# Kernel optimization log

Measured on AMD Instinct MI355X. Metric: run time of the kernel, lower is better.

## Reference

```python
import jax, jax.numpy as jnp
import numpy as np

EPS = 1e-05  # epsilon from __init__
K, D = 2048, 256  # codebook_size, embed dim (hardcoded in module)
B, T = 8, 8192


def setup_inputs() -> dict:
    key = jax.random.key(0)
    k1, k2, k3 = jax.random.split(key, 3)
    hidden_states = jax.random.normal(k1, (B, T, D), dtype=jnp.float32)
    embed_sum = jax.random.normal(k2, (K, D), dtype=jnp.float32)
    # cluster_usage starts as ones in the module; use positive random counts
    cluster_usage = jax.random.uniform(k3, (K,), dtype=jnp.float32) * 10.0 + 0.5
    return {"hidden_states": hidden_states, "embed_sum": embed_sum, "cluster_usage": cluster_usage}


def reference(hidden_states, embed_sum, cluster_usage):
    # embed property: embed_sum / clamp(cluster_usage, min=eps)[:, None]
    embed = embed_sum / jnp.clip(cluster_usage, EPS, None)[:, None]  # [K, D]

    shape = hidden_states.shape
    x = hidden_states.reshape(-1, shape[-1]).astype(jnp.float32)  # [N, D]

    x2 = jnp.sum(x * x, axis=-1, keepdims=True)        # [N, 1]
    e2 = jnp.sum(embed * embed, axis=-1)               # [K]
    d2 = x2 - 2.0 * (x @ embed.T) + e2[None, :]        # [N, K] -- the big intermediate

    embed_ind = jnp.argmin(d2, axis=-1).reshape(shape[:-1])  # [B, T]
    # decode: embedding lookup of selected codes
    quantized = jnp.take(embed, embed_ind, axis=0)            # [B, T, D]
    return embed_ind, quantized
```

## Files before the change

### kernel.cpp

```cpp
#include <hip/hip_runtime.h>
#include <hip/hip_bf16.h>


typedef float f32x4 __attribute__((ext_vector_type(4)));
typedef short s16x8 __attribute__((ext_vector_type(8)));

#define D_DIM 256
#define N_ROWS 65536
#define K_CODES 2048
#define VQ_EPS 1e-5f
#define DELTA 0.5f

__device__ __forceinline__ short bf16s(float f) {
    __hip_bfloat16 h = __float2bfloat16(f);
    return __builtin_bit_cast(short, h);
}
__device__ __forceinline__ unsigned fkey(float f) {
    unsigned u = __float_as_uint(f);
    return u ^ (unsigned)(((int)u >> 31) | (int)0x80000000);
}
__device__ __forceinline__ float funkey(unsigned k) {
    unsigned u = (k & 0x80000000u) ? (k ^ 0x80000000u) : ~k;
    return __uint_as_float(u);
}
__device__ __forceinline__ void gload16(const void* g, void* l) {
    __builtin_amdgcn_global_load_lds(
        (const __attribute__((address_space(1))) void*)g,
        (__attribute__((address_space(3))) void*)l, 16, 0, 0);
}

__device__ __forceinline__ void np_sumsq_16lane(const float* a, float* out, int g) {
#pragma clang fp contract(off)
    int j = g & 7, h = g >> 3;
    const float* p = a + h * 128;
    float t = p[j];
    float r = t * t;
#pragma unroll
    for (int i = 1; i < 16; ++i) { float v = p[j + 8 * i]; r += v * v; }
    r += __shfl_xor(r, 1);
    r += __shfl_xor(r, 2);
    r += __shfl_xor(r, 4);
    float other = __shfl_xor(r, 8);
    if (g == 0) *out = r + other;
}

__global__ void prep_codebook(const float* __restrict__ es, const float* __restrict__ us,
                              float* __restrict__ embed, unsigned short* __restrict__ eswz,
                              float* __restrict__ e2) {
    __shared__ float le[8][256];
    const int tid = threadIdx.x;
    const int rloc = tid >> 5, idx = tid & 31;
    const int r = blockIdx.x * 8 + rloc;
    const float u = fmaxf(us[r], VQ_EPS);
    f32x4 v0 = *(const f32x4*)&es[r * D_DIM + idx * 8];
    f32x4 v1 = *(const f32x4*)&es[r * D_DIM + idx * 8 + 4];
    f32x4 e0, e1;
#pragma unroll
    for (int j = 0; j < 4; ++j) { e0[j] = v0[j] / u; e1[j] = v1[j] / u; }
    *(f32x4*)&embed[r * D_DIM + idx * 8] = e0;
    *(f32x4*)&embed[r * D_DIM + idx * 8 + 4] = e1;
    *(f32x4*)&le[rloc][idx * 8] = e0;
    *(f32x4*)&le[rloc][idx * 8 + 4] = e1;
    int kc = idx >> 2, ss = idx & 3;
    int sd = ss ^ ((r >> 1) & 3);
    s16x8 b;
#pragma unroll
    for (int j = 0; j < 4; ++j) { b[j] = bf16s(e0[j]); b[j + 4] = bf16s(e1[j]); }
    *(s16x8*)&eswz[r * 256 + kc * 32 + sd * 8] = b;
    __syncthreads();
    if (idx < 16) np_sumsq_16lane(&le[rloc][0], &e2[r], idx);
}

__global__ void prep_x(const float* __restrict__ x, unsigned short* __restrict__ dst,
                       float* __restrict__ x2) {
    int gid = blockIdx.x * 256 + threadIdx.x;
    int r = gid >> 5, idx = gid & 31;
    int kc = idx >> 2, s = idx & 3;
    int k0 = kc * 32 + (s ^ ((r >> 1) & 3)) * 8;
    const float* p = x + r * D_DIM + k0;
    s16x8 v;
#pragma unroll
    for (int j = 0; j < 8; ++j) v[j] = bf16s(p[j]);
    *(s16x8*)&dst[r * 256 + kc * 32 + s * 8] = v;
    if (idx < 16)
        np_sumsq_16lane(x + r * D_DIM, x2 + r, idx);
}

__launch_bounds__(256, 2)
__global__ void vq_scan(const unsigned short* __restrict__ xswz,
                        const unsigned short* __restrict__ eswz,
                        const float* __restrict__ e2, const float* __restrict__ x2,
                        unsigned* __restrict__ keys1, unsigned* __restrict__ keys2) {
    __shared__ __align__(16) short lds[2][2][4096];

    const int bid = blockIdx.x;
    const int swz = (bid & 7) * 1024 + (bid >> 3);
    const int mt = swz >> 4, nt = swz & 15;
    const int m_base = mt * 128, n_base = nt * 128;
    const int tid = threadIdx.x, lane = tid & 63, wid = tid >> 6;
    const int rb = wid * 32;
    const int l15 = lane & 15, lg = lane >> 4;

    f32x4 acc[2][8];
#pragma unroll
    for (int m = 0; m < 2; ++m)
#pragma unroll
        for (int n = 0; n < 8; ++n) { f32x4 z = {0.f, 0.f, 0.f, 0.f}; acc[m][n] = z; }

    auto stage = [&](int buf, int kc) {
#pragma unroll
        for (int i = 0; i < 2; ++i) {
            int off = i * 4096 + wid * 1024 + lane * 16;
            int row = off >> 6, slot = (off >> 4) & 3;
            gload16((const char*)xswz + (((size_t)(m_base + row)) << 9) + (kc << 6) + (slot << 4),
                    (char*)&lds[buf][0][0] + off);
            gload16((const char*)eswz + (((size_t)(n_base + row)) << 9) + (kc << 6) + (slot << 4),
                    (char*)&lds[buf][1][0] + off);
        }
    };
    auto compute = [&](int buf) {
        const short* A = &lds[buf][0][0];
        const short* B = &lds[buf][1][0];
        s16x8 af[2], bf[8];
#pragma unroll
        for (int m = 0; m < 2; ++m) {
            int R = rb + m * 16 + l15, s = lg ^ ((R >> 1) & 3);
            af[m] = *(const s16x8*)&A[R * 32 + s * 8];
        }
#pragma unroll
        for (int n = 0; n < 8; ++n) {
            int R = n * 16 + l15, s = lg ^ ((R >> 1) & 3);
            bf[n] = *(const s16x8*)&B[R * 32 + s * 8];
        }
#pragma unroll
        for (int m = 0; m < 2; ++m)
#pragma unroll
            for (int n = 0; n < 8; ++n)
                acc[m][n] = __builtin_amdgcn_mfma_f32_16x16x32_bf16(af[m], bf[n], acc[m][n], 0, 0, 0);
    };

    stage(0, 0);
    __syncthreads();
#pragma unroll 1
    for (int kc = 0; kc < 8; ++kc) {
        if (kc < 7) stage((kc + 1) & 1, kc + 1);
        compute(kc & 1);
        __syncthreads();
    }

    const int grow0 = m_base + rb + lg * 4;
    float e2v[8];
#pragma unroll
    for (int n = 0; n < 8; ++n) e2v[n] = e2[n_base + n * 16 + l15];

#pragma unroll
    for (int m = 0; m < 2; ++m) {
#pragma unroll
        for (int j = 0; j < 4; ++j) {
            int gr = grow0 + m * 16 + j;
            float x2v = x2[gr];
            unsigned k1 = 0xFFFFFFFFu, k2 = 0xFFFFFFFFu;
#pragma unroll
            for (int n = 0; n < 8; ++n) {
                float d2 = (x2v - 2.0f * acc[m][n][j]) + e2v[n];
                unsigned pk = (fkey(d2) & 0xFFFFF800u)
                              | (unsigned)(n_base + n * 16 + l15);
                unsigned lo = pk < k1 ? pk : k1;
                unsigned hi = pk < k1 ? k1 : pk;
                k2 = hi < k2 ? hi : k2;
                k1 = lo;
            }
#pragma unroll
            for (int s = 1; s < 16; s <<= 1) {
                unsigned o1 = __shfl_xor(k1, s);
                unsigned o2 = __shfl_xor(k2, s);
                unsigned lo = o1 < k1 ? o1 : k1;
                unsigned hi = o1 < k1 ? k1 : o1;
                unsigned m2 = o2 < k2 ? o2 : k2;
                k2 = hi < m2 ? hi : m2;
                k1 = lo;
            }
            if (l15 == 0) {
                keys1[gr * 16 + nt] = k1;
                keys2[gr * 16 + nt] = k2;
            }
        }
    }
}

__launch_bounds__(256, 4)
__global__ void vq_rescore(const float* __restrict__ x, const float* __restrict__ embed,
                           const float* __restrict__ e2, const float* __restrict__ x2,
                           const unsigned* __restrict__ keys1,
                           const unsigned* __restrict__ keys2,
                           const float* __restrict__ es, const float* __restrict__ us,
                           float* __restrict__ out) {
    __shared__ float lx[4][256];
    __shared__ float le[4][4][260];
    __shared__ int lcode[4][16];
    __shared__ int lnc[4];

    const int tid = threadIdx.x, w = tid >> 6, lane = tid & 63;
    const int r = blockIdx.x * 4 + w;
    const int t16 = lane & 15;
    const float x2v = x2[r];

    *(f32x4*)&lx[w][lane * 4] = *(const f32x4*)&x[r * D_DIM + lane * 4];

    unsigned key = keys1[r * 16 + t16];
    unsigned kd = key & 0xFFFFF800u;
    unsigned kmin = kd;
#pragma unroll
    for (int s = 1; s < 16; s <<= 1) {
        unsigned ok = __shfl_xor(kmin, s);
        kmin = ok < kmin ? ok : kmin;
    }
    const float thr = funkey(kmin) + DELTA;
    const float deq = funkey(kd);

    bool cand = (lane < 16) && (deq <= thr);
    bool resc = (lane < 16) &&
                (funkey(keys2[r * 16 + t16] & 0xFFFFF800u) <= thr);
    unsigned long long cmask = __ballot(cand);
    unsigned long long rmask = __ballot(resc);
    if (cand)
        lcode[w][__popcll(cmask & ((1ull << lane) - 1ull))] = (int)(key & 0x7FFu);
    if (lane == 0) lnc[w] = __popcll(cmask);
    __syncthreads();

    int gmax = lnc[0];
#pragma unroll
    for (int i = 1; i < 4; ++i) gmax = max(gmax, lnc[i]);
    gmax = (gmax + 3) >> 2;

    float bv = __builtin_inff();
    int bi = 0x7FFFFFFF;
    auto lexmin = [&](float d2, int code) {
        if (d2 < bv || (d2 == bv && code < bi)) { bv = d2; bi = code; }
    };

#pragma unroll 1
    for (int g = 0; g < gmax; ++g) {
        const int nc = lnc[w];
#pragma unroll
        for (int v = 0; v < 4; ++v) {
            int idx = g * 4 + v;
            if (idx < nc) {
                int code = lcode[w][idx];
                *(f32x4*)&le[w][v][lane * 4] =
                    *(const f32x4*)&embed[code * D_DIM + lane * 4];
            }
        }
        __syncthreads();
        int idx = g * 4 + lane;
        if (lane < 4 && idx < nc) {
            int code = lcode[w][idx];
            float t = 0.0f;
#pragma unroll 8
            for (int k4 = 0; k4 < 64; ++k4) {
                f32x4 a4 = *(const f32x4*)&lx[w][k4 * 4];
                f32x4 e4 = *(const f32x4*)&le[w][lane][k4 * 4];
                t = __builtin_fmaf(a4[0], e4[0], t);
                t = __builtin_fmaf(a4[1], e4[1], t);
                t = __builtin_fmaf(a4[2], e4[2], t);
                t = __builtin_fmaf(a4[3], e4[3], t);
            }
            lexmin((x2v - 2.0f * t) + e2[code], code);
        }
        __syncthreads();
    }

    while (rmask) {
        int t2 = __ffsll(rmask) - 1;
        rmask &= rmask - 1;
        int ca = t2 * 128 + lane, cb = ca + 64;
        float ta = 0.0f, tb = 0.0f;
#pragma unroll 8
        for (int k4 = 0; k4 < 64; ++k4) {
            f32x4 a4 = *(const f32x4*)&lx[w][k4 * 4];
            f32x4 ea = *(const f32x4*)&embed[ca * D_DIM + k4 * 4];
            f32x4 eb = *(const f32x4*)&embed[cb * D_DIM + k4 * 4];
            ta = __builtin_fmaf(a4[0], ea[0], ta);
            tb = __builtin_fmaf(a4[0], eb[0], tb);
            ta = __builtin_fmaf(a4[1], ea[1], ta);
            tb = __builtin_fmaf(a4[1], eb[1], tb);
            ta = __builtin_fmaf(a4[2], ea[2], ta);
            tb = __builtin_fmaf(a4[2], eb[2], tb);
            ta = __builtin_fmaf(a4[3], ea[3], ta);
            tb = __builtin_fmaf(a4[3], eb[3], tb);
        }
        lexmin((x2v - 2.0f * ta) + e2[ca], ca);
        lexmin((x2v - 2.0f * tb) + e2[cb], cb);
    }

#pragma unroll
    for (int s = 1; s < 64; s <<= 1) {
        float ov = __shfl_xor(bv, s);
        int oi = __shfl_xor(bi, s);
        if (ov < bv || (ov == bv && oi < bi)) { bv = ov; bi = oi; }
    }
    if (lane == 0) out[r] = (float)bi;

    float u = fmaxf(us[bi], VQ_EPS);
    f32x4 wv = *(const f32x4*)&es[bi * D_DIM + lane * 4];
    f32x4 o;
#pragma unroll
    for (int j = 0; j < 4; ++j) o[j] = wv[j] / u;
    *(f32x4*)&out[N_ROWS + r * D_DIM + lane * 4] = o;
}

extern "C" void kernel_launch(void* const* d_in, const int* in_sizes, int n_in,
                              void* d_out, int out_size, void* d_ws, size_t ws_size,
                              hipStream_t stream) {
    const float* x = (const float*)d_in[0];
    const float* es = (const float*)d_in[1];
    const float* us = (const float*)d_in[2];
    float* out = (float*)d_out;

    char* w = (char*)d_ws;
    unsigned short* xswz = (unsigned short*)(w);
    unsigned short* eswz = (unsigned short*)(w + 33554432);
    float* embed         = (float*)(w + 34603008);
    float* e2            = (float*)(w + 36700160);
    float* x2            = (float*)(w + 36708352);
    unsigned* keys1      = (unsigned*)(w + 36970496);
    unsigned* keys2      = (unsigned*)(w + 41164800);

    hipLaunchKernelGGL(prep_codebook, dim3(256), dim3(256), 0, stream,
                       es, us, embed, eswz, e2);
    hipLaunchKernelGGL(prep_x, dim3(8192), dim3(256), 0, stream, x, xswz, x2);
    hipLaunchKernelGGL(vq_scan, dim3(8192), dim3(256), 0, stream,
                       xswz, eswz, e2, x2, keys1, keys2);
    hipLaunchKernelGGL(vq_rescore, dim3(16384), dim3(256), 0, stream,
                       x, embed, e2, x2, keys1, keys2, es, us, out);
}
```

Before: 241.4 us.

## Switch scan to fp16 MFMA, keep top-4 per tile, drop rescore barriers

The coarse distance scan now converts x and the codebook to fp16 instead of bf16 and uses the f16 MFMA, so the approximate distances carry more mantissa bits. The rescore margin is halved to match. Each 128-code tile now keeps a sorted top-4 candidate list packed into one uint4, instead of top-2 in two arrays. This is meant to reduce both the exact candidate rescoring and the expensive full-tile fallback scans. The rescore kernel compacts up to 64 candidates per row with ballots, processes them 8 at a time, and removes the block-wide __syncthreads, relying on each wave touching only its own LDS slice. In exchange, key traffic doubles and each tile does a larger sorting network, and fp16 has narrower range than bf16.

New measurement: 229.3 us. 1.05x faster.

```diff
diff --git a/kernel.cpp b/kernel.cpp
--- a/kernel.cpp
+++ b/kernel.cpp
@@ -4,15 +4,16 @@
 
 typedef float f32x4 __attribute__((ext_vector_type(4)));
 typedef short s16x8 __attribute__((ext_vector_type(8)));
+typedef _Float16 h16x8 __attribute__((ext_vector_type(8)));
 
 #define D_DIM 256
 #define N_ROWS 65536
 #define K_CODES 2048
 #define VQ_EPS 1e-5f
-#define DELTA 0.5f
-
-__device__ __forceinline__ short bf16s(float f) {
-    __hip_bfloat16 h = __float2bfloat16(f);
+#define DELTA 0.25f
+
+__device__ __forceinline__ short f16s(float f) {
+    _Float16 h = (_Float16)f;
     return __builtin_bit_cast(short, h);
 }
 __device__ __forceinline__ unsigned fkey(float f) {
@@ -65,7 +66,7 @@
     int sd = ss ^ ((r >> 1) & 3);
     s16x8 b;
 #pragma unroll
-    for (int j = 0; j < 4; ++j) { b[j] = bf16s(e0[j]); b[j + 4] = bf16s(e1[j]); }
+    for (int j = 0; j < 4; ++j) { b[j] = f16s(e0[j]); b[j + 4] = f16s(e1[j]); }
     *(s16x8*)&eswz[r * 256 + kc * 32 + sd * 8] = b;
     __syncthreads();
     if (idx < 16) np_sumsq_16lane(&le[rloc][0], &e2[r], idx);
@@ -80,7 +81,7 @@
     const float* p = x + r * D_DIM + k0;
     s16x8 v;
 #pragma unroll
-    for (int j = 0; j < 8; ++j) v[j] = bf16s(p[j]);
+    for (int j = 0; j < 8; ++j) v[j] = f16s(p[j]);
     *(s16x8*)&dst[r * 256 + kc * 32 + s * 8] = v;
     if (idx < 16)
         np_sumsq_16lane(x + r * D_DIM, x2 + r, idx);
@@ -90,7 +91,7 @@
 __global__ void vq_scan(const unsigned short* __restrict__ xswz,
                         const unsigned short* __restrict__ eswz,
                         const float* __restrict__ e2, const float* __restrict__ x2,
-                        unsigned* __restrict__ keys1, unsigned* __restrict__ keys2) {
+                        uint4* __restrict__ keys) {
     __shared__ __align__(16) short lds[2][2][4096];
 
     const int bid = blockIdx.x;
@@ -121,22 +122,22 @@
     auto compute = [&](int buf) {
         const short* A = &lds[buf][0][0];
         const short* B = &lds[buf][1][0];
-        s16x8 af[2], bf[8];
+        h16x8 af[2], bf[8];
 #pragma unroll
         for (int m = 0; m < 2; ++m) {
             int R = rb + m * 16 + l15, s = lg ^ ((R >> 1) & 3);
-            af[m] = *(const s16x8*)&A[R * 32 + s * 8];
+            af[m] = __builtin_bit_cast(h16x8, *(const s16x8*)&A[R * 32 + s * 8]);
         }
 #pragma unroll
         for (int n = 0; n < 8; ++n) {
             int R = n * 16 + l15, s = lg ^ ((R >> 1) & 3);
-            bf[n] = *(const s16x8*)&B[R * 32 + s * 8];
+            bf[n] = __builtin_bit_cast(h16x8, *(const s16x8*)&B[R * 32 + s * 8]);
         }
 #pragma unroll
         for (int m = 0; m < 2; ++m)
 #pragma unroll
             for (int n = 0; n < 8; ++n)
-                acc[m][n] = __builtin_amdgcn_mfma_f32_16x16x32_bf16(af[m], bf[n], acc[m][n], 0, 0, 0);
+                acc[m][n] = __builtin_amdgcn_mfma_f32_16x16x32_f16(af[m], bf[n], acc[m][n], 0, 0, 0);
     };
 
     stage(0, 0);
@@ -160,29 +161,33 @@
             int gr = grow0 + m * 16 + j;
             float x2v = x2[gr];
             unsigned k1 = 0xFFFFFFFFu, k2 = 0xFFFFFFFFu;
+            unsigned k3 = 0xFFFFFFFFu, k4 = 0xFFFFFFFFu;
 #pragma unroll
             for (int n = 0; n < 8; ++n) {
                 float d2 = (x2v - 2.0f * acc[m][n][j]) + e2v[n];
                 unsigned pk = (fkey(d2) & 0xFFFFF800u)
                               | (unsigned)(n_base + n * 16 + l15);
-                unsigned lo = pk < k1 ? pk : k1;
-                unsigned hi = pk < k1 ? k1 : pk;
-                k2 = hi < k2 ? hi : k2;
-                k1 = lo;
+                unsigned a = min(pk, k1), b = max(pk, k1); k1 = a;
+                a = min(b, k2); b = max(b, k2); k2 = a;
+                a = min(b, k3); b = max(b, k3); k3 = a;
+                k4 = min(b, k4);
             }
 #pragma unroll
             for (int s = 1; s < 16; s <<= 1) {
-                unsigned o1 = __shfl_xor(k1, s);
-                unsigned o2 = __shfl_xor(k2, s);
-                unsigned lo = o1 < k1 ? o1 : k1;
-                unsigned hi = o1 < k1 ? k1 : o1;
-                unsigned m2 = o2 < k2 ? o2 : k2;
-                k2 = hi < m2 ? hi : m2;
-                k1 = lo;
+                unsigned o1 = __shfl_xor(k1, s), o2 = __shfl_xor(k2, s);
+                unsigned o3 = __shfl_xor(k3, s), o4 = __shfl_xor(k4, s);
+                unsigned c1 = min(k1, o4), c2 = min(k2, o3);
+                unsigned c3 = min(k3, o2), c4 = min(k4, o1);
+                unsigned t;
+                t = min(c1, c3); c3 = max(c1, c3); c1 = t;
+                t = min(c2, c4); c4 = max(c2, c4); c2 = t;
+                t = min(c1, c2); c2 = max(c1, c2); c1 = t;
+                t = min(c3, c4); c4 = max(c3, c4); c3 = t;
+                k1 = c1; k2 = c2; k3 = c3; k4 = c4;
             }
             if (l15 == 0) {
-                keys1[gr * 16 + nt] = k1;
-                keys2[gr * 16 + nt] = k2;
+                uint4 kq; kq.x = k1; kq.y = k2; kq.z = k3; kq.w = k4;
+                keys[gr * 16 + nt] = kq;
             }
         }
     }
@@ -191,47 +196,41 @@
 __launch_bounds__(256, 4)
 __global__ void vq_rescore(const float* __restrict__ x, const float* __restrict__ embed,
                            const float* __restrict__ e2, const float* __restrict__ x2,
-                           const unsigned* __restrict__ keys1,
-                           const unsigned* __restrict__ keys2,
+                           const uint4* __restrict__ keys,
                            const float* __restrict__ es, const float* __restrict__ us,
                            float* __restrict__ out) {
     __shared__ float lx[4][256];
-    __shared__ float le[4][4][260];
-    __shared__ int lcode[4][16];
-    __shared__ int lnc[4];
+    __shared__ float le[4][8][260];
+    __shared__ int lcode[4][64];
 
     const int tid = threadIdx.x, w = tid >> 6, lane = tid & 63;
     const int r = blockIdx.x * 4 + w;
     const int t16 = lane & 15;
     const float x2v = x2[r];
+    const unsigned long long lt = (1ull << lane) - 1ull;
 
     *(f32x4*)&lx[w][lane * 4] = *(const f32x4*)&x[r * D_DIM + lane * 4];
 
-    unsigned key = keys1[r * 16 + t16];
-    unsigned kd = key & 0xFFFFF800u;
-    unsigned kmin = kd;
+    uint4 kq = keys[r * 16 + t16];
+    unsigned kmin = kq.x & 0xFFFFF800u;
 #pragma unroll
     for (int s = 1; s < 16; s <<= 1) {
         unsigned ok = __shfl_xor(kmin, s);
         kmin = ok < kmin ? ok : kmin;
     }
     const float thr = funkey(kmin) + DELTA;
-    const float deq = funkey(kd);
-
-    bool cand = (lane < 16) && (deq <= thr);
-    bool resc = (lane < 16) &&
-                (funkey(keys2[r * 16 + t16] & 0xFFFFF800u) <= thr);
-    unsigned long long cmask = __ballot(cand);
+
+    unsigned sv[4] = {kq.x, kq.y, kq.z, kq.w};
+    int nc = 0;
+#pragma unroll
+    for (int s = 0; s < 4; ++s) {
+        bool v = (lane < 16) && (funkey(sv[s] & 0xFFFFF800u) <= thr);
+        unsigned long long b = __ballot(v);
+        if (v) lcode[w][nc + __popcll(b & lt)] = (int)(sv[s] & 0x7FFu);
+        nc += (int)__popcll(b);
+    }
+    bool resc = (lane < 16) && (funkey(kq.w & 0xFFFFF800u) <= thr);
     unsigned long long rmask = __ballot(resc);
-    if (cand)
-        lcode[w][__popcll(cmask & ((1ull << lane) - 1ull))] = (int)(key & 0x7FFu);
-    if (lane == 0) lnc[w] = __popcll(cmask);
-    __syncthreads();
-
-    int gmax = lnc[0];
-#pragma unroll
-    for (int i = 1; i < 4; ++i) gmax = max(gmax, lnc[i]);
-    gmax = (gmax + 3) >> 2;
 
     float bv = __builtin_inff();
     int bi = 0x7FFFFFFF;
@@ -240,20 +239,18 @@
     };
 
 #pragma unroll 1
-    for (int g = 0; g < gmax; ++g) {
-        const int nc = lnc[w];
-#pragma unroll
-        for (int v = 0; v < 4; ++v) {
-            int idx = g * 4 + v;
+    for (int g = 0; g < (nc + 7) >> 3; ++g) {
+#pragma unroll
+        for (int v = 0; v < 8; ++v) {
+            int idx = g * 8 + v;
             if (idx < nc) {
                 int code = lcode[w][idx];
                 *(f32x4*)&le[w][v][lane * 4] =
                     *(const f32x4*)&embed[code * D_DIM + lane * 4];
             }
         }
-        __syncthreads();
-        int idx = g * 4 + lane;
-        if (lane < 4 && idx < nc) {
+        int idx = g * 8 + lane;
+        if (lane < 8 && idx < nc) {
             int code = lcode[w][idx];
             float t = 0.0f;
 #pragma unroll 8
@@ -267,7 +264,6 @@
             }
             lexmin((x2v - 2.0f * t) + e2[code], code);
         }
-        __syncthreads();
     }
 
     while (rmask) {
@@ -323,14 +319,13 @@
     float* embed         = (float*)(w + 34603008);
     float* e2            = (float*)(w + 36700160);
     float* x2            = (float*)(w + 36708352);
-    unsigned* keys1      = (unsigned*)(w + 36970496);
-    unsigned* keys2      = (unsigned*)(w + 41164800);
+    uint4* keys          = (uint4*)(w + 36970496);
 
     hipLaunchKernelGGL(prep_codebook, dim3(256), dim3(256), 0, stream,
                        es, us, embed, eswz, e2);
     hipLaunchKernelGGL(prep_x, dim3(8192), dim3(256), 0, stream, x, xswz, x2);
     hipLaunchKernelGGL(vq_scan, dim3(8192), dim3(256), 0, stream,
-                       xswz, eswz, e2, x2, keys1, keys2);
+                       xswz, eswz, e2, x2, keys);
     hipLaunchKernelGGL(vq_rescore, dim3(16384), dim3(256), 0, stream,
-                       x, embed, e2, x2, keys1, keys2, es, us, out);
-}
+                       x, embed, e2, x2, keys, es, us, out);
+}
```
